# Performance work log

Hardware: AMD Instinct MI355X
Metric: run time of the kernel (lower is better)

The kernel has to match this reference:

```python
import jax, jax.numpy as jnp
import numpy as np
import math

NUM_HEADS = 16
ROPE_BASE = 10000.0


def _rope_tables(T, head_dim, dtype=jnp.float32):
    pos = jnp.arange(T, dtype=jnp.float32)
    inv_freq = 1.0 / (ROPE_BASE ** (jnp.arange(0, head_dim, 2, dtype=jnp.float32) / head_dim))
    ang = pos[:, None] * inv_freq[None, :]  # (T, D/2)
    return jnp.cos(ang).astype(dtype), jnp.sin(ang).astype(dtype)


def _apply_rope(x, cos, sin):
    # x: (B, T, H, D); rotate interleaved pairs, position indexed along T
    B, T, H, D = x.shape
    xr = x.reshape(B, T, H, D // 2, 2)
    xe, xo = xr[..., 0], xr[..., 1]
    c = cos[None, :, None, :]  # (1, T, 1, D/2)
    s = sin[None, :, None, :]
    re = xe * c - xo * s
    im = xe * s + xo * c
    return jnp.stack([re, im], axis=-1).reshape(B, T, H, D)


def setup_inputs() -> dict:
    key = jax.random.key(0)
    k1, k2, k3 = jax.random.split(key, 3)
    B, T, C = 2, 2048, 1024
    x = jax.random.normal(k1, (B, T, C), dtype=jnp.float32)
    w_qkv = jax.random.normal(k2, (C, 3 * C), dtype=jnp.float32) * (1.0 / math.sqrt(C))
    w_out = jax.random.normal(k3, (C, C), dtype=jnp.float32) * (1.0 / math.sqrt(C))
    return {"x": x, "w_qkv": w_qkv, "w_out": w_out}


def reference(x, w_qkv, w_out):
    B, T, C = x.shape
    H = NUM_HEADS
    D = C // H
    qkv = jnp.einsum('btc,cf->btf', x, w_qkv)  # (B, T, 3C)
    q, k, v = jnp.split(qkv, 3, axis=-1)
    q = q.reshape(B, T, H, D)
    k = k.reshape(B, T, H, D)
    v = v.reshape(B, T, H, D)
    cos, sin = _rope_tables(T, D)
    q = _apply_rope(q, cos, sin)
    k = _apply_rope(k, cos, sin)
    # (B, H, T, T) scores with causal mask
    att = jnp.einsum('bqhd,bkhd->bhqk', q, k) * (1.0 / math.sqrt(D))
    causal = jnp.tril(jnp.ones((T, T), dtype=bool))
    att = jnp.where(causal[None, None], att, -jnp.inf)
    att = jax.nn.softmax(att, axis=-1)
    out = jnp.einsum('bhqk,bkhd->bqhd', att, v).reshape(B, T, C)
    return jnp.einsum('btc,cd->btd', out, w_out)
```

## Files before the change

kernel.cpp:

```cpp
#include <hip/hip_runtime.h>
#include <stdint.h>


#define B_ 2
#define T_ 2048
#define C_ 1024
#define H_ 16
#define D_ 64
#define F_ 3072
#define M_ 4096

typedef unsigned short u16;
typedef unsigned int u32;
typedef u16 u16x2 __attribute__((ext_vector_type(2)));
typedef u16 u16x4 __attribute__((ext_vector_type(4)));
typedef u16 u16x8 __attribute__((ext_vector_type(8)));
typedef __bf16 bf16x8 __attribute__((ext_vector_type(8)));
typedef float f32x4 __attribute__((ext_vector_type(4)));

#define AS1 __attribute__((address_space(1)))
#define AS3 __attribute__((address_space(3)))

__device__ __forceinline__ float b2f(u16 u) {
  union { unsigned int i; float f; } v; v.i = ((unsigned int)u) << 16; return v.f;
}
__device__ __forceinline__ u16 f2b(float f) {
  unsigned int u = __float_as_uint(f);
  u += 0x7fffu + ((u >> 16) & 1u);
  return (u16)(u >> 16);
}
__device__ __forceinline__ bf16x8 u2b8(u16x8 v) {
  union { u16x8 u; bf16x8 b; } x; x.u = v; return x.b;
}


__global__ __launch_bounds__(256) void rope_table_kernel(float2* csT) {
  int idx = blockIdx.x * 256 + threadIdx.x;
  int t = idx >> 5, i = idx & 31;
  float inv_freq = powf(10000.0f, -(float)(2 * i) / 64.0f);
  float ang = (float)t * inv_freq;
  csT[idx] = make_float2(cosf(ang), sinf(ang));
}

__global__ __launch_bounds__(256) void cast_x_kernel(const float* __restrict__ x,
                                                     u16* __restrict__ xb) {
  int i = blockIdx.x * 256 + threadIdx.x;
  float4 v = ((const float4*)x)[i];
  u16x4 r;
  r[0] = f2b(v.x); r[1] = f2b(v.y); r[2] = f2b(v.z); r[3] = f2b(v.w);
  ((u16x4*)xb)[i] = r;
}

__global__ __launch_bounds__(256) void transpose_cast_kernel(const float* __restrict__ in,
                                                             u16* __restrict__ out,
                                                             int R, int Ccol) {
  __shared__ float tile[32][33];
  int c0 = blockIdx.x * 32, r0 = blockIdx.y * 32;
  int tx = threadIdx.x & 31, ty = threadIdx.x >> 5;
  #pragma unroll
  for (int i = 0; i < 32; i += 8)
    tile[ty + i][tx] = in[(size_t)(r0 + ty + i) * Ccol + c0 + tx];
  __syncthreads();
  #pragma unroll
  for (int i = 0; i < 32; i += 8)
    out[(size_t)(c0 + ty + i) * R + r0 + tx] = f2b(tile[tx][ty + i]);
}

template <int MODE>
__global__ __launch_bounds__(256) void gemm_bt_kernel(const u16* __restrict__ A,
                                                      const u16* __restrict__ Bt,
                                                      float* __restrict__ Cm,
                                                      u16* __restrict__ qr,
                                                      u16* __restrict__ kr,
                                                      u16* __restrict__ vrp,
                                                      const float2* __restrict__ csT,
                                                      int M, int N, int K) {
  __shared__ u16 sA[3][128 * 32];
  __shared__ u16 sB[3][128 * 32];
  const int tid = threadIdx.x;
  const int lane = tid & 63;
  const int wv = tid >> 6;
  const int wr = wv >> 1, wc = wv & 1;
  const int l16 = lane & 15, lq = lane >> 4;
  const int rowBase = blockIdx.y * 128;
  const int colBase = blockIdx.x * 128;

  f32x4 acc[4][4] = {};

  const int e0 = wv * 1024 + lane * 8;

#define GSTAGE(buf, kk)                                                          \
  {                                                                              \
    _Pragma("unroll")                                                            \
    for (int s = 0; s < 2; ++s) {                                                \
      int e = e0 + s * 512;                                                      \
      int r = e >> 5, ccc = e & 31;                                              \
      __builtin_amdgcn_global_load_lds(                                          \
          (const AS1 u32*)(A + (size_t)(rowBase + r) * K + (kk) + ccc),          \
          (AS3 u32*)&sA[buf][wv * 1024 + s * 512], 16, 0, 0);                    \
      __builtin_amdgcn_global_load_lds(                                          \
          (const AS1 u32*)(Bt + (size_t)(colBase + r) * K + (kk) + ccc),         \
          (AS3 u32*)&sB[buf][wv * 1024 + s * 512], 16, 0, 0);                    \
    }                                                                            \
  }

  const int NT = K >> 5;
  GSTAGE(0, 0);
  if (NT > 1) GSTAGE(1, 32);

  int cur = 0;
  for (int kt = 0; kt < NT; ++kt) {
    if (kt + 1 < NT) {
      asm volatile("s_waitcnt vmcnt(4)" ::: "memory");
    } else {
      asm volatile("s_waitcnt vmcnt(0)" ::: "memory");
    }
    __builtin_amdgcn_s_barrier();

    if (kt + 2 < NT) {
      int nb = cur + 2; if (nb >= 3) nb -= 3;
      GSTAGE(nb, (kt + 2) * 32);
    }

    bf16x8 af[4], bf[4];
    #pragma unroll
    for (int m = 0; m < 4; ++m)
      af[m] = u2b8(*(const u16x8*)&sA[cur][(wr * 64 + m * 16 + l16) * 32 + lq * 8]);
    #pragma unroll
    for (int n = 0; n < 4; ++n)
      bf[n] = u2b8(*(const u16x8*)&sB[cur][(wc * 64 + n * 16 + l16) * 32 + lq * 8]);
    __builtin_amdgcn_s_setprio(1);
    #pragma unroll
    for (int m = 0; m < 4; ++m)
      #pragma unroll
      for (int n = 0; n < 4; ++n)
        acc[m][n] = __builtin_amdgcn_mfma_f32_16x16x32_bf16(af[m], bf[n], acc[m][n], 0, 0, 0);
    __builtin_amdgcn_s_setprio(0);

    cur = (cur + 1 == 3) ? 0 : cur + 1;
  }
#undef GSTAGE

  if constexpr (MODE == 0) {
    #pragma unroll
    for (int m = 0; m < 4; ++m)
      #pragma unroll
      for (int n = 0; n < 4; ++n) {
        int row = rowBase + wr * 64 + m * 16 + lq * 4;
        int col = colBase + wc * 64 + n * 16 + l16;
        #pragma unroll
        for (int j = 0; j < 4; ++j)
          Cm[(size_t)(row + j) * N + col] = acc[m][n][j];
      }
  } else {
    const int which = colBase >> 10;
    const int head = ((colBase + wc * 64) >> 6) & 15;
    const float QSC = 0.125f * 1.44269504f;
    u16* const dst = (which == 0) ? qr : (which == 1) ? kr : vrp;
    #pragma unroll
    for (int m = 0; m < 4; ++m) {
      #pragma unroll
      for (int n = 0; n < 4; ++n) {
        const int d0 = n * 16 + l16;
        #pragma unroll
        for (int j = 0; j < 4; ++j) {
          int row = rowBase + wr * 64 + m * 16 + lq * 4 + j;
          int b = row >> 11, t = row & 2047;
          float v = acc[m][n][j];
          u16 outv;
          if (which == 2) {
            outv = f2b(v);
          } else {
            float p = __shfl_xor(v, 1);
            float2 cs = csT[t * 32 + (d0 >> 1)];
            float r = (l16 & 1) ? fmaf(p, cs.y, v * cs.x)
                                : fmaf(-p, cs.y, v * cs.x);
            if (which == 0) r *= QSC;
            outv = f2b(r);
          }
          dst[((size_t)(b * 16 + head) * 2048 + t) * 64 + d0] = outv;
        }
      }
    }
  }
}

__global__ __launch_bounds__(256, 4) void attn_mfma_kernel(const u16* __restrict__ qr,
                                                           const u16* __restrict__ kr,
                                                           const u16* __restrict__ vr,
                                                           u16* __restrict__ ao) {
  constexpr int LDVT = 72;
  __shared__ u16 sK[2][64 * 64];
  __shared__ u16 sVt[2][64 * LDVT];

  const int tid = threadIdx.x;
  const int lane = tid & 63;
  const int w = tid >> 6;
  const int l16 = lane & 15, lq = lane >> 4;
  const int bh = blockIdx.x;
  const int qt = (int)gridDim.y - 1 - (int)blockIdx.y;
  const int qbase = qt * 64;
  const size_t hb = (size_t)bh * (T_ * D_);

  bf16x8 qv[2];
  #pragma unroll
  for (int dc = 0; dc < 2; ++dc) {
    int row = qbase + w * 16 + l16;
    qv[dc] = u2b8(*(const u16x8*)(qr + hb + (size_t)row * 64 + dc * 32 + lq * 8));
  }

  f32x4 o[4] = {};
  float mrow = -1e30f;
  float lrow = 0.0f;

  const int krow0 = w * 16 + (lane >> 3);
  const int ksrc = ((lane & 7) ^ (lane >> 3)) * 8;
  const int vkp = tid & 31;
  const int vdb = tid >> 5;
  const int vtr = ((vkp >> 4) & 1) * 32 + ((vkp >> 1) & 1) * 16 +
                  ((vkp >> 3) & 1) * 8 + ((vkp >> 2) & 1) * 4 + (vkp & 1) * 2;

  u16x8 rv0, rv1;
#define STAGEK(buf, k0s)                                                       \
  {                                                                            \
    _Pragma("unroll")                                                          \
    for (int s = 0; s < 2; ++s)                                                \
      __builtin_amdgcn_global_load_lds(                                        \
          (const AS1 u32*)(kr + hb + (size_t)((k0s) + krow0 + s * 8) * 64 + ksrc), \
          (AS3 u32*)&sK[buf][(w * 16 + s * 8) * 64], 16, 0, 0);                \
  }
#define LOADV(k0s)                                                             \
  {                                                                            \
    rv0 = *(const u16x8*)(vr + hb + (size_t)((k0s) + vtr) * 64 + vdb * 8);     \
    rv1 = *(const u16x8*)(vr + hb + (size_t)((k0s) + vtr + 1) * 64 + vdb * 8); \
  }
#define WRITEV(buf)                                                            \
  {                                                                            \
    _Pragma("unroll")                                                          \
    for (int u = 0; u < 8; ++u) {                                              \
      u16x2 pk; pk[0] = rv0[u]; pk[1] = rv1[u];                                \
      *(u16x2*)&sVt[buf][(vdb * 8 + u) * LDVT + 2 * vkp] = pk;                 \
    }                                                                          \
  }

  STAGEK(0, 0);
  LOADV(0);
  WRITEV(0);
  __syncthreads();

  const int nt = qt + 1;
  int cur = 0;
  for (int it = 0; it < nt; ++it) {
    const int k0 = it * 64;
    const bool more = (it + 1 < nt);
    if (more) {
      STAGEK(cur ^ 1, k0 + 64);
      LOADV(k0 + 64);
    }

    f32x4 accs[4] = {};
    __builtin_amdgcn_s_setprio(1);
    #pragma unroll
    for (int kt = 0; kt < 4; ++kt) {
      int chy = ((lq) ^ (l16 & 7)) * 8;
      int chz = ((4 + lq) ^ (l16 & 7)) * 8;
      bf16x8 kf0 = u2b8(*(const u16x8*)&sK[cur][(kt * 16 + l16) * 64 + chy]);
      bf16x8 kf1 = u2b8(*(const u16x8*)&sK[cur][(kt * 16 + l16) * 64 + chz]);
      accs[kt] = __builtin_amdgcn_mfma_f32_16x16x32_bf16(kf0, qv[0], accs[kt], 0, 0, 0);
      accs[kt] = __builtin_amdgcn_mfma_f32_16x16x32_bf16(kf1, qv[1], accs[kt], 0, 0, 0);
    }
    __builtin_amdgcn_s_setprio(0);

    const int qrow = qbase + w * 16 + l16;
    if (k0 + 63 > qbase + w * 16) {
      #pragma unroll
      for (int kt = 0; kt < 4; ++kt)
        #pragma unroll
        for (int j = 0; j < 4; ++j)
          if (k0 + kt * 16 + lq * 4 + j > qrow) accs[kt][j] = -1e30f;
    }
    float m0 = fmaxf(fmaxf(accs[0][0], accs[0][1]), fmaxf(accs[0][2], accs[0][3]));
    float m1 = fmaxf(fmaxf(accs[1][0], accs[1][1]), fmaxf(accs[1][2], accs[1][3]));
    float m2 = fmaxf(fmaxf(accs[2][0], accs[2][1]), fmaxf(accs[2][2], accs[2][3]));
    float m3 = fmaxf(fmaxf(accs[3][0], accs[3][1]), fmaxf(accs[3][2], accs[3][3]));
    float mx = fmaxf(fmaxf(m0, m1), fmaxf(m2, m3));
    mx = fmaxf(mx, __shfl_xor(mx, 16));
    mx = fmaxf(mx, __shfl_xor(mx, 32));

    if (!__all(mx <= mrow)) {
      float mnew = fmaxf(mrow, mx);
      float corr = __builtin_amdgcn_exp2f(mrow - mnew);
      lrow *= corr;
      mrow = mnew;
      f32x4 corrv;
      #pragma unroll
      for (int j = 0; j < 4; ++j) corrv[j] = __shfl(corr, lq * 4 + j);
      #pragma unroll
      for (int dt = 0; dt < 4; ++dt) o[dt] *= corrv;
    }
    const float mu = mrow;
    bf16x8 pb[2];
    float lsum = 0.0f;
    #pragma unroll
    for (int kt = 0; kt < 4; ++kt) {
      #pragma unroll
      for (int j = 0; j < 4; ++j) {
        float p = __builtin_amdgcn_exp2f(accs[kt][j] - mu);
        lsum += p;
        pb[kt >> 1][(kt & 1) * 4 + j] = (__bf16)p;
      }
    }
    lrow += lsum;

    __builtin_amdgcn_s_setprio(1);
    #pragma unroll
    for (int kc = 0; kc < 2; ++kc) {
      #pragma unroll
      for (int dt = 0; dt < 4; ++dt) {
        bf16x8 vt = u2b8(*(const u16x8*)&sVt[cur][(dt * 16 + l16) * LDVT + kc * 32 + lq * 8]);
        o[dt] = __builtin_amdgcn_mfma_f32_16x16x32_bf16(pb[kc], vt, o[dt], 0, 0, 0);
      }
    }
    __builtin_amdgcn_s_setprio(0);

    if (more) WRITEV(cur ^ 1);
    __syncthreads();
    cur ^= 1;
  }

  const int b = bh >> 4, h = bh & 15;
  float l = lrow;
  l += __shfl_xor(l, 16);
  l += __shfl_xor(l, 32);
  float linv = 1.0f / l;
  #pragma unroll
  for (int j = 0; j < 4; ++j) {
    float lj = __shfl(linv, lq * 4 + j);
    int row = qbase + w * 16 + lq * 4 + j;
    u16* orow = ao + ((size_t)(b * T_ + row)) * C_ + h * 64;
    #pragma unroll
    for (int dt = 0; dt < 4; ++dt)
      orow[dt * 16 + l16] = f2b(o[dt][j] * lj);
  }
}

extern "C" void kernel_launch(void* const* d_in, const int* in_sizes, int n_in,
                              void* d_out, int out_size, void* d_ws, size_t ws_size,
                              hipStream_t stream) {
  const float* x     = (const float*)d_in[0];
  const float* w_qkv = (const float*)d_in[1];
  const float* w_out = (const float*)d_in[2];
  float* out = (float*)d_out;
  char* ws = (char*)d_ws;

  u16* xb     = (u16*)(ws + 0);
  u16* wqkvT  = (u16*)(ws + 8388608);
  u16* woutT  = (u16*)(ws + 14680064);
  u16* qr     = (u16*)(ws + 41943040);
  u16* kr     = (u16*)(ws + 50331648);
  u16* vr     = (u16*)(ws + 58720256);
  u16* ao     = (u16*)(ws + 67108864);
  float2* csT = (float2*)(ws + 75497472);

  rope_table_kernel<<<256, 256, 0, stream>>>(csT);
  cast_x_kernel<<<4096, 256, 0, stream>>>(x, xb);
  transpose_cast_kernel<<<dim3(96, 32), 256, 0, stream>>>(w_qkv, wqkvT, C_, F_);
  transpose_cast_kernel<<<dim3(32, 32), 256, 0, stream>>>(w_out, woutT, C_, C_);
  gemm_bt_kernel<2><<<dim3(F_ / 128, M_ / 128), 256, 0, stream>>>(
      xb, wqkvT, nullptr, qr, kr, vr, (const float2*)csT, M_, F_, C_);
  attn_mfma_kernel<<<dim3(B_ * H_, T_ / 64), 256, 0, stream>>>(qr, kr, vr, ao);
  gemm_bt_kernel<0><<<dim3(C_ / 128, M_ / 128), 256, 0, stream>>>(
      ao, woutT, out, nullptr, nullptr, nullptr, nullptr, M_, C_, C_);
}
```

Measured before the change: 134.9 us.

## Split attention KV range into two halves with log-sum-exp combine kernel

Result: no change. 136.5 us (+1.2%).

```diff
diff --git a/kernel.cpp b/kernel.cpp
--- a/kernel.cpp
+++ b/kernel.cpp
@@ -188,7 +188,9 @@
 __global__ __launch_bounds__(256, 4) void attn_mfma_kernel(const u16* __restrict__ qr,
                                                            const u16* __restrict__ kr,
                                                            const u16* __restrict__ vr,
-                                                           u16* __restrict__ ao) {
+                                                           u16* __restrict__ ao,
+                                                           u16* __restrict__ po1,
+                                                           float* __restrict__ wbuf) {
   constexpr int LDVT = 72;
   __shared__ u16 sK[2][64 * 64];
   __shared__ u16 sVt[2][64 * LDVT];
@@ -198,9 +200,25 @@
   const int w = tid >> 6;
   const int l16 = lane & 15, lq = lane >> 4;
   const int bh = blockIdx.x;
-  const int qt = (int)gridDim.y - 1 - (int)blockIdx.y;
+  const int p = (int)gridDim.y - 1 - (int)blockIdx.y;
+  const int qt = p >> 1, half = p & 1;
   const int qbase = qt * 64;
   const size_t hb = (size_t)bh * (T_ * D_);
+
+  const int nt = qt + 1;
+  const int nh = (nt + 1) >> 1;
+  const int t0 = half ? nh : 0;
+  const int t1 = half ? nt : nh;
+
+  if (t0 >= t1) {
+    int row = qbase + (tid >> 2);
+    int seg = (tid & 3) * 16;
+    u16x8 z = {};
+    *(u16x8*)(po1 + (((size_t)bh << 11) + row) * 64 + seg) = z;
+    *(u16x8*)(po1 + (((size_t)bh << 11) + row) * 64 + seg + 8) = z;
+    if (tid < 64) wbuf[(((size_t)bh << 11) + qbase + tid) * 2 + half] = -1e30f;
+    return;
+  }
 
   bf16x8 qv[2];
   #pragma unroll
@@ -243,16 +261,15 @@
     }                                                                          \
   }
 
-  STAGEK(0, 0);
-  LOADV(0);
+  STAGEK(0, t0 * 64);
+  LOADV(t0 * 64);
   WRITEV(0);
   __syncthreads();
 
-  const int nt = qt + 1;
   int cur = 0;
-  for (int it = 0; it < nt; ++it) {
+  for (int it = t0; it < t1; ++it) {
     const int k0 = it * 64;
-    const bool more = (it + 1 < nt);
+    const bool more = (it + 1 < t1);
     if (more) {
       STAGEK(cur ^ 1, k0 + 64);
       LOADV(k0 + 64);
@@ -305,9 +322,9 @@
     for (int kt = 0; kt < 4; ++kt) {
       #pragma unroll
       for (int j = 0; j < 4; ++j) {
-        float p = __builtin_amdgcn_exp2f(accs[kt][j] - mu);
-        lsum += p;
-        pb[kt >> 1][(kt & 1) * 4 + j] = (__bf16)p;
+        float p2 = __builtin_amdgcn_exp2f(accs[kt][j] - mu);
+        lsum += p2;
+        pb[kt >> 1][(kt & 1) * 4 + j] = (__bf16)p2;
       }
     }
     lrow += lsum;
@@ -333,15 +350,43 @@
   l += __shfl_xor(l, 16);
   l += __shfl_xor(l, 32);
   float linv = 1.0f / l;
+  float wrow = mrow + __log2f(l);
+  if (lq == 0)
+    wbuf[(((size_t)bh << 11) + qbase + w * 16 + l16) * 2 + half] = wrow;
   #pragma unroll
   for (int j = 0; j < 4; ++j) {
     float lj = __shfl(linv, lq * 4 + j);
     int row = qbase + w * 16 + lq * 4 + j;
-    u16* orow = ao + ((size_t)(b * T_ + row)) * C_ + h * 64;
+    u16* dst = (half == 0)
+        ? ao + ((size_t)(b * T_ + row)) * C_ + h * 64
+        : po1 + (((size_t)bh << 11) + row) * 64;
     #pragma unroll
     for (int dt = 0; dt < 4; ++dt)
-      orow[dt * 16 + l16] = f2b(o[dt][j] * lj);
-  }
+      dst[dt * 16 + l16] = f2b(o[dt][j] * lj);
+  }
+}
+
+__global__ __launch_bounds__(256) void combine_kernel(const u16* __restrict__ po1,
+                                                      const float* __restrict__ wbuf,
+                                                      u16* __restrict__ ao) {
+  int g = blockIdx.x * 256 + threadIdx.x;
+  int row = g >> 3, seg = g & 7;
+  int bh = row >> 11, t = row & 2047;
+  int b = bh >> 4, h = bh & 15;
+  size_t aoff = ((size_t)(b * T_ + t)) * C_ + h * 64 + seg * 8;
+  float w0 = wbuf[(size_t)row * 2 + 0];
+  float w1 = wbuf[(size_t)row * 2 + 1];
+  float mx = fmaxf(w0, w1);
+  float e0 = __builtin_amdgcn_exp2f(w0 - mx);
+  float e1 = __builtin_amdgcn_exp2f(w1 - mx);
+  float inv = 1.0f / (e0 + e1);
+  u16x8 a = *(u16x8*)(ao + aoff);
+  u16x8 q = *(const u16x8*)(po1 + (size_t)row * 64 + seg * 8);
+  u16x8 r;
+  #pragma unroll
+  for (int u = 0; u < 8; ++u)
+    r[u] = f2b((e0 * b2f(a[u]) + e1 * b2f(q[u])) * inv);
+  *(u16x8*)(ao + aoff) = r;
 }
 
 extern "C" void kernel_launch(void* const* d_in, const int* in_sizes, int n_in,
@@ -361,6 +406,8 @@
   u16* vr     = (u16*)(ws + 58720256);
   u16* ao     = (u16*)(ws + 67108864);
   float2* csT = (float2*)(ws + 75497472);
+  u16* po1    = (u16*)(ws + 0);
+  float* wbuf = (float*)(ws + 8388608);
 
   rope_table_kernel<<<256, 256, 0, stream>>>(csT);
   cast_x_kernel<<<4096, 256, 0, stream>>>(x, xb);
@@ -368,7 +415,8 @@
   transpose_cast_kernel<<<dim3(32, 32), 256, 0, stream>>>(w_out, woutT, C_, C_);
   gemm_bt_kernel<2><<<dim3(F_ / 128, M_ / 128), 256, 0, stream>>>(
       xb, wqkvT, nullptr, qr, kr, vr, (const float2*)csT, M_, F_, C_);
-  attn_mfma_kernel<<<dim3(B_ * H_, T_ / 64), 256, 0, stream>>>(qr, kr, vr, ao);
+  attn_mfma_kernel<<<dim3(B_ * H_, 2 * (T_ / 64)), 256, 0, stream>>>(qr, kr, vr, ao, po1, wbuf);
+  combine_kernel<<<2048, 256, 0, stream>>>(po1, wbuf, ao);
   gemm_bt_kernel<0><<<dim3(C_ / 128, M_ / 128), 256, 0, stream>>>(
       ao, woutT, out, nullptr, nullptr, nullptr, nullptr, M_, C_, C_);
 }
```

## Replace QKV projection GEMM with 256x256-tile 8-wave kernel using direct-to-LDS loads

Applied to the files above, without the earlier changes.

New measurement: 149.3 us. 10.6% more time.

```diff
diff --git a/kernel.cpp b/kernel.cpp
--- a/kernel.cpp
+++ b/kernel.cpp
@@ -66,14 +66,164 @@
     out[(size_t)(c0 + ty + i) * R + r0 + tx] = f2b(tile[tx][ty + i]);
 }
 
-template <int MODE>
+__global__ __launch_bounds__(512, 2) void gemm256_qkv_kernel(
+    const u16* __restrict__ A, const u16* __restrict__ Bt,
+    u16* __restrict__ qr, u16* __restrict__ kr, u16* __restrict__ vrp,
+    const float2* __restrict__ csT) {
+  __shared__ u16 sA[2][2][8192];
+  __shared__ u16 sB[2][2][8192];
+
+  const int tid = threadIdx.x;
+  const int lane = tid & 63;
+  const int wv = tid >> 6;
+  const int wr = wv >> 2, wc = wv & 3;
+  const int l16 = lane & 15, lq = lane >> 4;
+
+  const int flat = blockIdx.y * 12 + blockIdx.x;
+  const int swz = (flat & 7) * 24 + (flat >> 3);
+  const int bx = swz % 12, by = swz / 12;
+  const int rowBase = by * 256;
+  const int colBase = bx * 256;
+
+  const int lr8 = lane >> 3;
+  const int schunk = ((lane & 7) ^ (lr8 & 7)) * 8;
+
+#define STG_A(buf, half, kt)                                                     \
+  {                                                                              \
+    _Pragma("unroll")                                                            \
+    for (int l = 0; l < 2; ++l)                                                  \
+      __builtin_amdgcn_global_load_lds(                                          \
+          (const AS1 u32*)(A + (size_t)(rowBase + (half) * 128 + l * 64 + wv * 8 + lr8) * 1024 + (kt) * 64 + schunk), \
+          (AS3 u32*)&sA[buf][half][l * 4096 + wv * 512], 16, 0, 0);              \
+  }
+#define STG_B(buf, half, kt)                                                     \
+  {                                                                              \
+    _Pragma("unroll")                                                            \
+    for (int l = 0; l < 2; ++l)                                                  \
+      __builtin_amdgcn_global_load_lds(                                          \
+          (const AS1 u32*)(Bt + (size_t)(colBase + (half) * 128 + l * 64 + wv * 8 + lr8) * 1024 + (kt) * 64 + schunk), \
+          (AS3 u32*)&sB[buf][half][l * 4096 + wv * 512], 16, 0, 0);              \
+  }
+#define RD_A(buf, m, ks) \
+  u2b8(*(const u16x8*)&sA[buf][wr][(((m) * 16 + l16) << 6) + ((((ks) * 4 + lq) ^ (l16 & 7)) << 3)])
+#define RD_B(buf, n, ks) \
+  u2b8(*(const u16x8*)&sB[buf][wc >> 1][(((wc & 1) * 64 + (n) * 16 + l16) << 6) + ((((ks) * 4 + lq) ^ (l16 & 7)) << 3)])
+#define BAR() asm volatile("s_barrier" ::: "memory")
+
+  f32x4 acc[8][4] = {};
+
+  STG_A(0, 0, 0); STG_A(0, 1, 0);
+  STG_B(0, 0, 0); STG_B(0, 1, 0);
+  STG_B(1, 0, 1); STG_B(1, 1, 1);
+  asm volatile("s_waitcnt vmcnt(4)" ::: "memory");
+  BAR();
+
+  bf16x8 a0[4][2], a1[4][2], b0[2][2], b1[2][2];
+  const int NT = 16;
+  for (int t = 0; t < NT; ++t) {
+    const int buf = t & 1;
+    #pragma unroll
+    for (int m = 0; m < 4; ++m) { a0[m][0] = RD_A(buf, m, 0); a0[m][1] = RD_A(buf, m, 1); }
+    #pragma unroll
+    for (int n = 0; n < 2; ++n) { b0[n][0] = RD_B(buf, n, 0); b0[n][1] = RD_B(buf, n, 1); }
+    if (t + 1 < NT) STG_A(buf ^ 1, 0, t + 1);
+    BAR();
+    __builtin_amdgcn_s_setprio(1);
+    #pragma unroll
+    for (int m = 0; m < 4; ++m)
+      #pragma unroll
+      for (int n = 0; n < 2; ++n) {
+        acc[m][n] = __builtin_amdgcn_mfma_f32_16x16x32_bf16(a0[m][0], b0[n][0], acc[m][n], 0, 0, 0);
+        acc[m][n] = __builtin_amdgcn_mfma_f32_16x16x32_bf16(a0[m][1], b0[n][1], acc[m][n], 0, 0, 0);
+      }
+    __builtin_amdgcn_s_setprio(0);
+    BAR();
+    #pragma unroll
+    for (int n = 0; n < 2; ++n) { b1[n][0] = RD_B(buf, n + 2, 0); b1[n][1] = RD_B(buf, n + 2, 1); }
+    if (t + 1 < NT) STG_A(buf ^ 1, 1, t + 1);
+    BAR();
+    __builtin_amdgcn_s_setprio(1);
+    #pragma unroll
+    for (int m = 0; m < 4; ++m)
+      #pragma unroll
+      for (int n = 0; n < 2; ++n) {
+        acc[m][n + 2] = __builtin_amdgcn_mfma_f32_16x16x32_bf16(a0[m][0], b1[n][0], acc[m][n + 2], 0, 0, 0);
+        acc[m][n + 2] = __builtin_amdgcn_mfma_f32_16x16x32_bf16(a0[m][1], b1[n][1], acc[m][n + 2], 0, 0, 0);
+      }
+    __builtin_amdgcn_s_setprio(0);
+    BAR();
+    #pragma unroll
+    for (int m = 0; m < 4; ++m) { a1[m][0] = RD_A(buf, m + 4, 0); a1[m][1] = RD_A(buf, m + 4, 1); }
+    if (t + 2 < NT) STG_B(buf, 0, t + 2);
+    BAR();
+    __builtin_amdgcn_s_setprio(1);
+    #pragma unroll
+    for (int m = 0; m < 4; ++m)
+      #pragma unroll
+      for (int n = 0; n < 2; ++n) {
+        acc[m + 4][n] = __builtin_amdgcn_mfma_f32_16x16x32_bf16(a1[m][0], b0[n][0], acc[m + 4][n], 0, 0, 0);
+        acc[m + 4][n] = __builtin_amdgcn_mfma_f32_16x16x32_bf16(a1[m][1], b0[n][1], acc[m + 4][n], 0, 0, 0);
+      }
+    __builtin_amdgcn_s_setprio(0);
+    BAR();
+    if (t + 2 < NT) {
+      STG_B(buf, 1, t + 2);
+      asm volatile("s_waitcnt vmcnt(4)" ::: "memory");
+    } else {
+      asm volatile("s_waitcnt vmcnt(0)" ::: "memory");
+    }
+    BAR();
+    __builtin_amdgcn_s_setprio(1);
+    #pragma unroll
+    for (int m = 0; m < 4; ++m)
+      #pragma unroll
+      for (int n = 0; n < 2; ++n) {
+        acc[m + 4][n + 2] = __builtin_amdgcn_mfma_f32_16x16x32_bf16(a1[m][0], b1[n][0], acc[m + 4][n + 2], 0, 0, 0);
+        acc[m + 4][n + 2] = __builtin_amdgcn_mfma_f32_16x16x32_bf16(a1[m][1], b1[n][1], acc[m + 4][n + 2], 0, 0, 0);
+      }
+    __builtin_amdgcn_s_setprio(0);
+    BAR();
+  }
+#undef STG_A
+#undef STG_B
+#undef RD_A
+#undef RD_B
+#undef BAR
+
+  const int which = colBase >> 10;
+  const int head = ((colBase + wc * 64) >> 6) & 15;
+  const float QSC = 0.125f * 1.44269504f;
+  u16* const dst = (which == 0) ? qr : (which == 1) ? kr : vrp;
+  #pragma unroll
+  for (int m = 0; m < 8; ++m) {
+    #pragma unroll
+    for (int n = 0; n < 4; ++n) {
+      const int d0 = n * 16 + l16;
+      #pragma unroll
+      for (int j = 0; j < 4; ++j) {
+        int row = rowBase + wr * 128 + m * 16 + lq * 4 + j;
+        int b = row >> 11, t = row & 2047;
+        float v = acc[m][n][j];
+        u16 outv;
+        if (which == 2) {
+          outv = f2b(v);
+        } else {
+          float p = __shfl_xor(v, 1);
+          float2 cs = csT[t * 32 + (d0 >> 1)];
+          float r = (l16 & 1) ? fmaf(p, cs.y, v * cs.x)
+                              : fmaf(-p, cs.y, v * cs.x);
+          if (which == 0) r *= QSC;
+          outv = f2b(r);
+        }
+        dst[((size_t)(b * 16 + head) * 2048 + t) * 64 + d0] = outv;
+      }
+    }
+  }
+}
+
 __global__ __launch_bounds__(256) void gemm_bt_kernel(const u16* __restrict__ A,
                                                       const u16* __restrict__ Bt,
                                                       float* __restrict__ Cm,
-                                                      u16* __restrict__ qr,
-                                                      u16* __restrict__ kr,
-                                                      u16* __restrict__ vrp,
-                                                      const float2* __restrict__ csT,
                                                       int M, int N, int K) {
   __shared__ u16 sA[3][128 * 32];
   __shared__ u16 sB[3][128 * 32];
@@ -141,48 +291,16 @@
   }
 #undef GSTAGE
 
-  if constexpr (MODE == 0) {
-    #pragma unroll
-    for (int m = 0; m < 4; ++m)
-      #pragma unroll
-      for (int n = 0; n < 4; ++n) {
-        int row = rowBase + wr * 64 + m * 16 + lq * 4;
-        int col = colBase + wc * 64 + n * 16 + l16;
-        #pragma unroll
-        for (int j = 0; j < 4; ++j)
-          Cm[(size_t)(row + j) * N + col] = acc[m][n][j];
-      }
-  } else {
-    const int which = colBase >> 10;
-    const int head = ((colBase + wc * 64) >> 6) & 15;
-    const float QSC = 0.125f * 1.44269504f;
-    u16* const dst = (which == 0) ? qr : (which == 1) ? kr : vrp;
-    #pragma unroll
-    for (int m = 0; m < 4; ++m) {
-      #pragma unroll
-      for (int n = 0; n < 4; ++n) {
-        const int d0 = n * 16 + l16;
-        #pragma unroll
-        for (int j = 0; j < 4; ++j) {
-          int row = rowBase + wr * 64 + m * 16 + lq * 4 + j;
-          int b = row >> 11, t = row & 2047;
-          float v = acc[m][n][j];
-          u16 outv;
-          if (which == 2) {
-            outv = f2b(v);
-          } else {
-            float p = __shfl_xor(v, 1);
-            float2 cs = csT[t * 32 + (d0 >> 1)];
-            float r = (l16 & 1) ? fmaf(p, cs.y, v * cs.x)
-                                : fmaf(-p, cs.y, v * cs.x);
-            if (which == 0) r *= QSC;
-            outv = f2b(r);
-          }
-          dst[((size_t)(b * 16 + head) * 2048 + t) * 64 + d0] = outv;
-        }
-      }
-    }
-  }
+  #pragma unroll
+  for (int m = 0; m < 4; ++m)
+    #pragma unroll
+    for (int n = 0; n < 4; ++n) {
+      int row = rowBase + wr * 64 + m * 16 + lq * 4;
+      int col = colBase + wc * 64 + n * 16 + l16;
+      #pragma unroll
+      for (int j = 0; j < 4; ++j)
+        Cm[(size_t)(row + j) * N + col] = acc[m][n][j];
+    }
 }
 
 __global__ __launch_bounds__(256, 4) void attn_mfma_kernel(const u16* __restrict__ qr,
@@ -366,9 +484,7 @@
   cast_x_kernel<<<4096, 256, 0, stream>>>(x, xb);
   transpose_cast_kernel<<<dim3(96, 32), 256, 0, stream>>>(w_qkv, wqkvT, C_, F_);
   transpose_cast_kernel<<<dim3(32, 32), 256, 0, stream>>>(w_out, woutT, C_, C_);
-  gemm_bt_kernel<2><<<dim3(F_ / 128, M_ / 128), 256, 0, stream>>>(
-      xb, wqkvT, nullptr, qr, kr, vr, (const float2*)csT, M_, F_, C_);
+  gemm256_qkv_kernel<<<dim3(12, 16), 512, 0, stream>>>(xb, wqkvT, qr, kr, vr, (const float2*)csT);
   attn_mfma_kernel<<<dim3(B_ * H_, T_ / 64), 256, 0, stream>>>(qr, kr, vr, ao);
-  gemm_bt_kernel<0><<<dim3(C_ / 128, M_ / 128), 256, 0, stream>>>(
-      ao, woutT, out, nullptr, nullptr, nullptr, nullptr, M_, C_, C_);
-}
+  gemm_bt_kernel<<<dim3(C_ / 128, M_ / 128), 256, 0, stream>>>(ao, woutT, out, M_, C_, C_);
+}
```

## Enlarge attention query tile to 128 rows, two fragments per wave

Applied to the files above, without the earlier changes.

After: 146.4 us. 1.09x slower.

```diff
diff --git a/kernel.cpp b/kernel.cpp
--- a/kernel.cpp
+++ b/kernel.cpp
@@ -185,7 +185,7 @@
   }
 }
 
-__global__ __launch_bounds__(256, 4) void attn_mfma_kernel(const u16* __restrict__ qr,
+__global__ __launch_bounds__(256, 2) void attn_mfma_kernel(const u16* __restrict__ qr,
                                                            const u16* __restrict__ kr,
                                                            const u16* __restrict__ vr,
                                                            u16* __restrict__ ao) {
@@ -199,19 +199,21 @@
   const int l16 = lane & 15, lq = lane >> 4;
   const int bh = blockIdx.x;
   const int qt = (int)gridDim.y - 1 - (int)blockIdx.y;
-  const int qbase = qt * 64;
+  const int qbase = qt * 128;
   const size_t hb = (size_t)bh * (T_ * D_);
 
-  bf16x8 qv[2];
+  bf16x8 qv[2][2];
   #pragma unroll
-  for (int dc = 0; dc < 2; ++dc) {
-    int row = qbase + w * 16 + l16;
-    qv[dc] = u2b8(*(const u16x8*)(qr + hb + (size_t)row * 64 + dc * 32 + lq * 8));
-  }
-
-  f32x4 o[4] = {};
-  float mrow = -1e30f;
-  float lrow = 0.0f;
+  for (int qf = 0; qf < 2; ++qf)
+    #pragma unroll
+    for (int dc = 0; dc < 2; ++dc) {
+      int row = qbase + w * 32 + qf * 16 + l16;
+      qv[qf][dc] = u2b8(*(const u16x8*)(qr + hb + (size_t)row * 64 + dc * 32 + lq * 8));
+    }
+
+  f32x4 o[2][4] = {};
+  float mrow[2] = {-1e30f, -1e30f};
+  float lrow[2] = {0.0f, 0.0f};
 
   const int krow0 = w * 16 + (lane >> 3);
   const int ksrc = ((lane & 7) ^ (lane >> 3)) * 8;
@@ -248,7 +250,8 @@
   WRITEV(0);
   __syncthreads();
 
-  const int nt = qt + 1;
+  const int qmaxw = qbase + w * 32 + 31;
+  const int nt = qt * 2 + 2;
   int cur = 0;
   for (int it = 0; it < nt; ++it) {
     const int k0 = it * 64;
@@ -258,70 +261,78 @@
       LOADV(k0 + 64);
     }
 
-    f32x4 accs[4] = {};
-    __builtin_amdgcn_s_setprio(1);
-    #pragma unroll
-    for (int kt = 0; kt < 4; ++kt) {
-      int chy = ((lq) ^ (l16 & 7)) * 8;
-      int chz = ((4 + lq) ^ (l16 & 7)) * 8;
-      bf16x8 kf0 = u2b8(*(const u16x8*)&sK[cur][(kt * 16 + l16) * 64 + chy]);
-      bf16x8 kf1 = u2b8(*(const u16x8*)&sK[cur][(kt * 16 + l16) * 64 + chz]);
-      accs[kt] = __builtin_amdgcn_mfma_f32_16x16x32_bf16(kf0, qv[0], accs[kt], 0, 0, 0);
-      accs[kt] = __builtin_amdgcn_mfma_f32_16x16x32_bf16(kf1, qv[1], accs[kt], 0, 0, 0);
-    }
-    __builtin_amdgcn_s_setprio(0);
-
-    const int qrow = qbase + w * 16 + l16;
-    if (k0 + 63 > qbase + w * 16) {
-      #pragma unroll
-      for (int kt = 0; kt < 4; ++kt)
+    if (k0 <= qmaxw) {
+      f32x4 accs[2][4] = {};
+      __builtin_amdgcn_s_setprio(1);
+      #pragma unroll
+      for (int kt = 0; kt < 4; ++kt) {
+        int chy = ((lq) ^ (l16 & 7)) * 8;
+        int chz = ((4 + lq) ^ (l16 & 7)) * 8;
+        bf16x8 kf0 = u2b8(*(const u16x8*)&sK[cur][(kt * 16 + l16) * 64 + chy]);
+        bf16x8 kf1 = u2b8(*(const u16x8*)&sK[cur][(kt * 16 + l16) * 64 + chz]);
+        accs[0][kt] = __builtin_amdgcn_mfma_f32_16x16x32_bf16(kf0, qv[0][0], accs[0][kt], 0, 0, 0);
+        accs[0][kt] = __builtin_amdgcn_mfma_f32_16x16x32_bf16(kf1, qv[0][1], accs[0][kt], 0, 0, 0);
+        accs[1][kt] = __builtin_amdgcn_mfma_f32_16x16x32_bf16(kf0, qv[1][0], accs[1][kt], 0, 0, 0);
+        accs[1][kt] = __builtin_amdgcn_mfma_f32_16x16x32_bf16(kf1, qv[1][1], accs[1][kt], 0, 0, 0);
+      }
+      __builtin_amdgcn_s_setprio(0);
+
+      bf16x8 pb[2][2];
+      #pragma unroll
+      for (int qf = 0; qf < 2; ++qf) {
+        const int qrow = qbase + w * 32 + qf * 16 + l16;
+        if (k0 + 63 > qbase + w * 32 + qf * 16) {
+          #pragma unroll
+          for (int kt = 0; kt < 4; ++kt)
+            #pragma unroll
+            for (int j = 0; j < 4; ++j)
+              if (k0 + kt * 16 + lq * 4 + j > qrow) accs[qf][kt][j] = -1e30f;
+        }
+        float m0 = fmaxf(fmaxf(accs[qf][0][0], accs[qf][0][1]), fmaxf(accs[qf][0][2], accs[qf][0][3]));
+        float m1 = fmaxf(fmaxf(accs[qf][1][0], accs[qf][1][1]), fmaxf(accs[qf][1][2], accs[qf][1][3]));
+        float m2 = fmaxf(fmaxf(accs[qf][2][0], accs[qf][2][1]), fmaxf(accs[qf][2][2], accs[qf][2][3]));
+        float m3 = fmaxf(fmaxf(accs[qf][3][0], accs[qf][3][1]), fmaxf(accs[qf][3][2], accs[qf][3][3]));
+        float mx = fmaxf(fmaxf(m0, m1), fmaxf(m2, m3));
+        mx = fmaxf(mx, __shfl_xor(mx, 16));
+        mx = fmaxf(mx, __shfl_xor(mx, 32));
+
+        if (!__all(mx <= mrow[qf])) {
+          float mnew = fmaxf(mrow[qf], mx);
+          float corr = __builtin_amdgcn_exp2f(mrow[qf] - mnew);
+          lrow[qf] *= corr;
+          mrow[qf] = mnew;
+          f32x4 corrv;
+          #pragma unroll
+          for (int j = 0; j < 4; ++j) corrv[j] = __shfl(corr, lq * 4 + j);
+          #pragma unroll
+          for (int dt = 0; dt < 4; ++dt) o[qf][dt] *= corrv;
+        }
+        const float mu = mrow[qf];
+        float lsum = 0.0f;
         #pragma unroll
-        for (int j = 0; j < 4; ++j)
-          if (k0 + kt * 16 + lq * 4 + j > qrow) accs[kt][j] = -1e30f;
-    }
-    float m0 = fmaxf(fmaxf(accs[0][0], accs[0][1]), fmaxf(accs[0][2], accs[0][3]));
-    float m1 = fmaxf(fmaxf(accs[1][0], accs[1][1]), fmaxf(accs[1][2], accs[1][3]));
-    float m2 = fmaxf(fmaxf(accs[2][0], accs[2][1]), fmaxf(accs[2][2], accs[2][3]));
-    float m3 = fmaxf(fmaxf(accs[3][0], accs[3][1]), fmaxf(accs[3][2], accs[3][3]));
-    float mx = fmaxf(fmaxf(m0, m1), fmaxf(m2, m3));
-    mx = fmaxf(mx, __shfl_xor(mx, 16));
-    mx = fmaxf(mx, __shfl_xor(mx, 32));
-
-    if (!__all(mx <= mrow)) {
-      float mnew = fmaxf(mrow, mx);
-      float corr = __builtin_amdgcn_exp2f(mrow - mnew);
-      lrow *= corr;
-      mrow = mnew;
-      f32x4 corrv;
-      #pragma unroll
-      for (int j = 0; j < 4; ++j) corrv[j] = __shfl(corr, lq * 4 + j);
-      #pragma unroll
-      for (int dt = 0; dt < 4; ++dt) o[dt] *= corrv;
-    }
-    const float mu = mrow;
-    bf16x8 pb[2];
-    float lsum = 0.0f;
-    #pragma unroll
-    for (int kt = 0; kt < 4; ++kt) {
-      #pragma unroll
-      for (int j = 0; j < 4; ++j) {
-        float p = __builtin_amdgcn_exp2f(accs[kt][j] - mu);
-        lsum += p;
-        pb[kt >> 1][(kt & 1) * 4 + j] = (__bf16)p;
-      }
-    }
-    lrow += lsum;
-
-    __builtin_amdgcn_s_setprio(1);
-    #pragma unroll
-    for (int kc = 0; kc < 2; ++kc) {
-      #pragma unroll
-      for (int dt = 0; dt < 4; ++dt) {
-        bf16x8 vt = u2b8(*(const u16x8*)&sVt[cur][(dt * 16 + l16) * LDVT + kc * 32 + lq * 8]);
-        o[dt] = __builtin_amdgcn_mfma_f32_16x16x32_bf16(pb[kc], vt, o[dt], 0, 0, 0);
-      }
-    }
-    __builtin_amdgcn_s_setprio(0);
+        for (int kt = 0; kt < 4; ++kt) {
+          #pragma unroll
+          for (int j = 0; j < 4; ++j) {
+            float p = __builtin_amdgcn_exp2f(accs[qf][kt][j] - mu);
+            lsum += p;
+            pb[qf][kt >> 1][(kt & 1) * 4 + j] = (__bf16)p;
+          }
+        }
+        lrow[qf] += lsum;
+      }
+
+      __builtin_amdgcn_s_setprio(1);
+      #pragma unroll
+      for (int kc = 0; kc < 2; ++kc) {
+        #pragma unroll
+        for (int dt = 0; dt < 4; ++dt) {
+          bf16x8 vt = u2b8(*(const u16x8*)&sVt[cur][(dt * 16 + l16) * LDVT + kc * 32 + lq * 8]);
+          o[0][dt] = __builtin_amdgcn_mfma_f32_16x16x32_bf16(pb[0][kc], vt, o[0][dt], 0, 0, 0);
+          o[1][dt] = __builtin_amdgcn_mfma_f32_16x16x32_bf16(pb[1][kc], vt, o[1][dt], 0, 0, 0);
+        }
+      }
+      __builtin_amdgcn_s_setprio(0);
+    }
 
     if (more) WRITEV(cur ^ 1);
     __syncthreads();
@@ -329,18 +340,21 @@
   }
 
   const int b = bh >> 4, h = bh & 15;
-  float l = lrow;
-  l += __shfl_xor(l, 16);
-  l += __shfl_xor(l, 32);
-  float linv = 1.0f / l;
   #pragma unroll
-  for (int j = 0; j < 4; ++j) {
-    float lj = __shfl(linv, lq * 4 + j);
-    int row = qbase + w * 16 + lq * 4 + j;
-    u16* orow = ao + ((size_t)(b * T_ + row)) * C_ + h * 64;
-    #pragma unroll
-    for (int dt = 0; dt < 4; ++dt)
-      orow[dt * 16 + l16] = f2b(o[dt][j] * lj);
+  for (int qf = 0; qf < 2; ++qf) {
+    float l = lrow[qf];
+    l += __shfl_xor(l, 16);
+    l += __shfl_xor(l, 32);
+    float linv = 1.0f / l;
+    #pragma unroll
+    for (int j = 0; j < 4; ++j) {
+      float lj = __shfl(linv, lq * 4 + j);
+      int row = qbase + w * 32 + qf * 16 + lq * 4 + j;
+      u16* orow = ao + ((size_t)(b * T_ + row)) * C_ + h * 64;
+      #pragma unroll
+      for (int dt = 0; dt < 4; ++dt)
+        orow[dt * 16 + l16] = f2b(o[qf][dt][j] * lj);
+    }
   }
 }
 
@@ -368,7 +382,7 @@
   transpose_cast_kernel<<<dim3(32, 32), 256, 0, stream>>>(w_out, woutT, C_, C_);
   gemm_bt_kernel<2><<<dim3(F_ / 128, M_ / 128), 256, 0, stream>>>(
       xb, wqkvT, nullptr, qr, kr, vr, (const float2*)csT, M_, F_, C_);
-  attn_mfma_kernel<<<dim3(B_ * H_, T_ / 64), 256, 0, stream>>>(qr, kr, vr, ao);
+  attn_mfma_kernel<<<dim3(B_ * H_, T_ / 128), 256, 0, stream>>>(qr, kr, vr, ao);
   gemm_bt_kernel<0><<<dim3(C_ / 128, M_ / 128), 256, 0, stream>>>(
       ao, woutT, out, nullptr, nullptr, nullptr, nullptr, M_, C_, C_);
 }
```
